# Kernel tuning notes

Measured on AMD Instinct MI355X. Metric: run time of the kernel, lower is better.

Reference implementation:

```python
import jax, jax.numpy as jnp
import numpy as np

BIG_NEG = -1000000000.0
B, N, X, D = 16, 32, 36, 2048
H = 512

def setup_inputs() -> dict:
    key = jax.random.key(0)
    ks = jax.random.split(key, 16)
    inp = {
        'fc_feats_target': jax.random.normal(ks[0], (B, 1, D), jnp.float32),
        'fc_feats_distr': jax.random.normal(ks[1], (B, N, D), jnp.float32),
        'att_feats_target': jax.random.normal(ks[2], (B, 1, X, D), jnp.float32),
        'att_feats_distr': jax.random.normal(ks[3], (B, N, X, D), jnp.float32),
        'att_masks_target': jax.random.randint(ks[4], (B, 1, X), 0, 2, jnp.int32),
        'att_masks_distr': jax.random.randint(ks[5], (B, N, X), 0, 2, jnp.int32),
        # scorer MLP params: Linear(2D->H), Linear(H->1)
        'W1': jax.random.normal(ks[6], (2 * D, H), jnp.float32) * 0.02,
        'b1': jnp.zeros((H,), jnp.float32),
        'W2': jax.random.normal(ks[7], (H, 1), jnp.float32) * 0.02,
        'b2': jnp.zeros((1,), jnp.float32),
        # bilinear weight, initialized to identity as in the module
        'Wbil': jnp.eye(D, dtype=jnp.float32),
        # object_scorer MLP params
        'oW1': jax.random.normal(ks[8], (2 * D, H), jnp.float32) * 0.02,
        'ob1': jnp.zeros((H,), jnp.float32),
        'oW2': jax.random.normal(ks[9], (H, 1), jnp.float32) * 0.02,
        'ob2': jnp.zeros((1,), jnp.float32),
    }
    return inp

def _mlp(x, W1, b1, W2, b2):
    h = jax.nn.relu(x @ W1 + b1)
    return (h @ W2 + b2)[..., 0]  # squeeze(-1)

def reference(fc_feats_target, fc_feats_distr, att_feats_target, att_feats_distr,
              att_masks_target, att_masks_distr,
              W1, b1, W2, b2, Wbil, oW1, ob1, oW2, ob2):
    # base scorer on global (fc) features
    ft = jnp.broadcast_to(fc_feats_target, fc_feats_distr.shape)  # [B,N,D]
    cat_feats = jnp.concatenate([ft, fc_feats_distr], axis=-1)    # [B,N,2D]
    scores = _mlp(cat_feats, W1, b1, W2, b2)                      # [B,N]

    # bilinear compatibility: einsum('bixd,biye,de->bixy') with target broadcast over i
    tproj = jnp.einsum('bxd,de->bxe', att_feats_target[:, 0], Wbil)        # [B,X,D]
    inners = jnp.einsum('bxd,biyd->bixy', tproj, att_feats_distr)          # [B,N,X,Y]

    mask_outer = (att_masks_target[:, 0][:, None, :, None]
                  * att_masks_distr[:, :, None, :])                        # [B,N,X,Y]
    inners = jnp.where(mask_outer > 0, inners, BIG_NEG)

    target_weights = jax.nn.softmax(jnp.max(inners, axis=3), axis=-1)      # [B,N,X]
    distr_weights = jax.nn.softmax(jnp.max(inners, axis=2), axis=-1)       # [B,N,Y]

    target_feats = jnp.einsum('bxd,bix->bid', att_feats_target[:, 0], target_weights)
    distr_feats = jnp.einsum('biyd,biy->bid', att_feats_distr, distr_weights)

    cat_att = jnp.concatenate([target_feats, distr_feats], axis=-1)        # [B,N,2D]
    scores = scores + _mlp(cat_att, oW1, ob1, oW2, ob2)

    return jax.nn.log_softmax(scores, axis=-1)  # [B,N]
```

## Files before the change

### kernel.cpp

```cpp
#include <hip/hip_runtime.h>
#include <math.h>

#define D_   2048
#define H_   512
#define K2D  4096
#define X_   36
#define NCOL 1152

#define Z_MLP 32
#define Z_TP  8
#define Z_S   4

#define O_A   0u
#define O_B   9437184u
#define O_SB  11534336u
#define O_SO  11534848u

#define SP_PLANE 663552u

typedef __attribute__((ext_vector_type(8))) short bf8_t;
typedef __attribute__((ext_vector_type(4))) float f4_t;

__device__ __forceinline__ unsigned short f2bf(float f) {
  unsigned u = __float_as_uint(f);
  unsigned r = u + 0x7FFFu + ((u >> 16) & 1u);
  return (unsigned short)(r >> 16);
}
__device__ __forceinline__ float bf2f(unsigned short h) {
  return __uint_as_float(((unsigned)h) << 16);
}

#define TSTR 40

__device__ __forceinline__ void cvt8(unsigned short* Hp, unsigned short* Lp,
                                     float4 a, float4 b) {
  __align__(16) unsigned short h[8], l[8];
  float x[8] = {a.x, a.y, a.z, a.w, b.x, b.y, b.z, b.w};
  #pragma unroll
  for (int j = 0; j < 8; j++) {
    h[j] = f2bf(x[j]);
    l[j] = f2bf(x[j] - bf2f(h[j]));
  }
  *(bf8_t*)Hp = *(bf8_t*)&h[0];
  *(bf8_t*)Lp = *(bf8_t*)&l[0];
}

__global__ __launch_bounds__(256, 4) void gemm_mfma64(
    const float* __restrict__ A, const float* __restrict__ A2,
    const float* __restrict__ Bm, float* __restrict__ Cpart,
    int M, int N, int K, int kchunk, int amode)
{
  __shared__ __align__(16) unsigned short AsH[64 * TSTR], AsL[64 * TSTR];
  __shared__ __align__(16) unsigned short BsH[64 * TSTR], BsL[64 * TSTR];
  const int t  = threadIdx.x;
  const int m0 = blockIdx.y << 6;
  const int n0 = blockIdx.x << 6;
  const int k0 = blockIdx.z * kchunk;
  const int kend = k0 + kchunk;
  const int w  = t >> 6;
  const int ln = t & 15;
  const int qd = (t >> 4) & 3;
  const int wm = (w >> 1) << 5;
  const int wn = (w & 1) << 5;
  const int a_row = t >> 2;
  const int a_kq  = (t & 3) << 3;
  const int b_col = t & 63;
  const int b_kq  = (t >> 6) << 3;

  f4_t acc[2][2];
  #pragma unroll
  for (int i = 0; i < 2; i++)
    #pragma unroll
    for (int j = 0; j < 2; j++) acc[i][j] = (f4_t)0.f;

  float4 pa0, pa1;
  float  pb[8];

  auto loadA = [&](int kb) {
    int gr = m0 + a_row;
    int gk = kb + a_kq;
    pa0 = make_float4(0.f, 0.f, 0.f, 0.f);
    pa1 = pa0;
    if (gr < M) {
      const float* src;
      if (amode == 0) src = A + (size_t)gr * K + gk;
      else src = (gk < 2048) ? (A  + ((size_t)(gr >> 5) << 11) + gk)
                             : (A2 + ((size_t)gr << 11) + (gk - 2048));
      pa0 = *(const float4*)src;
      pa1 = *(const float4*)(src + 4);
    }
  };
  auto loadB = [&](int kb) {
    #pragma unroll
    for (int j = 0; j < 8; j++)
      pb[j] = Bm[(size_t)(kb + b_kq + j) * N + n0 + b_col];
  };

  loadA(k0); loadB(k0);

  for (int kb = k0; kb < kend; kb += 32) {
    __syncthreads();
    cvt8(&AsH[a_row * TSTR + a_kq], &AsL[a_row * TSTR + a_kq], pa0, pa1);
    cvt8(&BsH[b_col * TSTR + b_kq], &BsL[b_col * TSTR + b_kq],
         make_float4(pb[0], pb[1], pb[2], pb[3]),
         make_float4(pb[4], pb[5], pb[6], pb[7]));
    __syncthreads();
    if (kb + 32 < kend) { loadA(kb + 32); loadB(kb + 32); }
    bf8_t ah[2], al[2], bh[2], bl[2];
    #pragma unroll
    for (int fm = 0; fm < 2; fm++) {
      int r = (wm + (fm << 4) + ln) * TSTR + (qd << 3);
      ah[fm] = *(const bf8_t*)&AsH[r];
      al[fm] = *(const bf8_t*)&AsL[r];
    }
    #pragma unroll
    for (int fn = 0; fn < 2; fn++) {
      int r = (wn + (fn << 4) + ln) * TSTR + (qd << 3);
      bh[fn] = *(const bf8_t*)&BsH[r];
      bl[fn] = *(const bf8_t*)&BsL[r];
    }
    #pragma unroll
    for (int fm = 0; fm < 2; fm++)
      #pragma unroll
      for (int fn = 0; fn < 2; fn++) {
        acc[fm][fn] = __builtin_amdgcn_mfma_f32_16x16x32_bf16(ah[fm], bh[fn], acc[fm][fn], 0, 0, 0);
        acc[fm][fn] = __builtin_amdgcn_mfma_f32_16x16x32_bf16(ah[fm], bl[fn], acc[fm][fn], 0, 0, 0);
        acc[fm][fn] = __builtin_amdgcn_mfma_f32_16x16x32_bf16(al[fm], bh[fn], acc[fm][fn], 0, 0, 0);
      }
  }
  float* Cz = Cpart + (size_t)blockIdx.z * M * N;
  #pragma unroll
  for (int fm = 0; fm < 2; fm++) {
    #pragma unroll
    for (int reg = 0; reg < 4; reg++) {
      int gr = m0 + wm + (fm << 4) + (qd << 2) + reg;
      if (gr < M) {
        #pragma unroll
        for (int fn = 0; fn < 2; fn++)
          Cz[(size_t)gr * N + n0 + wn + (fn << 4) + ln] = acc[fm][fn][reg];
      }
    }
  }
}

__global__ __launch_bounds__(256) void reduce_tp(
    const float* __restrict__ tpp, float* __restrict__ tproj)
{
  int idx = blockIdx.x * 256 + threadIdx.x;
  const float4* p = (const float4*)tpp;
  float4 a = p[idx];
  #pragma unroll
  for (int z = 1; z < Z_TP; z++) {
    float4 b = p[idx + (size_t)z * 294912];
    a.x += b.x; a.y += b.y; a.z += b.z; a.w += b.w;
  }
  ((float4*)tproj)[idx] = a;
}

__global__ __launch_bounds__(256, 4) void sgemm36_mfma(
    const float* __restrict__ tproj, const float* __restrict__ attd,
    float* __restrict__ Spart, int kchunk)
{
  __shared__ __align__(16) unsigned short AsH[48 * TSTR], AsL[48 * TSTR];
  __shared__ __align__(16) unsigned short BsH[64 * TSTR], BsL[64 * TSTR];
  const int t  = threadIdx.x;
  const int n0 = blockIdx.x << 6;
  const int b  = blockIdx.y;
  const int k0 = blockIdx.z * kchunk;
  const int kend = k0 + kchunk;
  const int w  = t >> 6;
  const int ln = t & 15;
  const int qd = (t >> 4) & 3;
  const float* Ab = tproj + (size_t)b * X_ * D_;
  const float* Bb = attd  + (size_t)b * NCOL * D_;
  const int a_row = t >> 2;
  const int a_kq  = (t & 3) << 3;
  const int b_col = t & 63;
  const int b_kq  = (t >> 6) << 3;

  f4_t acc[3];
  #pragma unroll
  for (int i = 0; i < 3; i++) acc[i] = (f4_t)0.f;

  float4 pa0, pa1, pb0, pb1;

  auto loadA = [&](int kb) {
    pa0 = make_float4(0.f, 0.f, 0.f, 0.f);
    pa1 = pa0;
    if (a_row < X_) {
      const float* src = Ab + (size_t)a_row * D_ + kb + a_kq;
      pa0 = *(const float4*)src;
      pa1 = *(const float4*)(src + 4);
    }
  };
  auto loadB = [&](int kb) {
    const float* src = Bb + (size_t)(n0 + b_col) * D_ + kb + b_kq;
    pb0 = *(const float4*)src;
    pb1 = *(const float4*)(src + 4);
  };

  loadA(k0); loadB(k0);

  for (int kb = k0; kb < kend; kb += 32) {
    __syncthreads();
    if (a_row < 48)
      cvt8(&AsH[a_row * TSTR + a_kq], &AsL[a_row * TSTR + a_kq], pa0, pa1);
    cvt8(&BsH[b_col * TSTR + b_kq], &BsL[b_col * TSTR + b_kq], pb0, pb1);
    __syncthreads();
    if (kb + 32 < kend) { loadA(kb + 32); loadB(kb + 32); }
    bf8_t ah[3], al[3], bh, bl;
    #pragma unroll
    for (int fm = 0; fm < 3; fm++) {
      int r = ((fm << 4) + ln) * TSTR + (qd << 3);
      ah[fm] = *(const bf8_t*)&AsH[r];
      al[fm] = *(const bf8_t*)&AsL[r];
    }
    {
      int r = ((w << 4) + ln) * TSTR + (qd << 3);
      bh = *(const bf8_t*)&BsH[r];
      bl = *(const bf8_t*)&BsL[r];
    }
    #pragma unroll
    for (int fm = 0; fm < 3; fm++) {
      acc[fm] = __builtin_amdgcn_mfma_f32_16x16x32_bf16(ah[fm], bh, acc[fm], 0, 0, 0);
      acc[fm] = __builtin_amdgcn_mfma_f32_16x16x32_bf16(ah[fm], bl, acc[fm], 0, 0, 0);
      acc[fm] = __builtin_amdgcn_mfma_f32_16x16x32_bf16(al[fm], bh, acc[fm], 0, 0, 0);
    }
  }
  float* Sz = Spart + (size_t)blockIdx.z * SP_PLANE + (size_t)b * X_ * NCOL;
  #pragma unroll
  for (int fm = 0; fm < 3; fm++) {
    #pragma unroll
    for (int reg = 0; reg < 4; reg++) {
      int x = (fm << 4) + (qd << 2) + reg;
      if (x < X_)
        Sz[(size_t)x * NCOL + n0 + (w << 4) + ln] = acc[fm][reg];
    }
  }
}

__global__ __launch_bounds__(256) void mlp_tail_z(
    const float* __restrict__ hp, const float* __restrict__ b1,
    const float* __restrict__ w2, const float* __restrict__ b2,
    float* __restrict__ out)
{
  int row = blockIdx.x;
  int t   = threadIdx.x;
  float v = 0.f;
  #pragma unroll
  for (int q = 0; q < 2; q++) {
    int h = t + (q << 8);
    float s = 0.f;
    #pragma unroll
    for (int z = 0; z < Z_MLP; z++)
      s += hp[(size_t)z * (H_ * 512) + (size_t)row * H_ + h];
    s += b1[h];
    v += fmaxf(s, 0.f) * w2[h];
  }
  #pragma unroll
  for (int off = 32; off > 0; off >>= 1) v += __shfl_down(v, off, 64);
  __shared__ float red[4];
  if ((t & 63) == 0) red[t >> 6] = v;
  __syncthreads();
  if (t == 0) out[row] = red[0] + red[1] + red[2] + red[3] + b2[0];
}

__global__ __launch_bounds__(256) void attn_fused(
    const float* __restrict__ Spart, const int* __restrict__ amt,
    const int* __restrict__ amd, const float* __restrict__ attt,
    const float* __restrict__ attd, float* __restrict__ cat)
{
  __shared__ float Sm[36 * 37];
  __shared__ int   mtv[36], mdv[36];
  __shared__ float mrow[36], mcol[36], twl[36], dwl[36];
  int bi = blockIdx.x;
  int b  = bi >> 5;
  int i  = bi & 31;
  int t  = threadIdx.x;
  if (t < 36) { mtv[t] = amt[b * 36 + t]; mdv[t] = amd[bi * 36 + t]; }
  __syncthreads();
  for (int f = t; f < 324; f += 256) {
    int x  = f / 9;
    int yq = (f - x * 9) << 2;
    size_t o = (((size_t)b * X_ + x) * NCOL + i * 36 + yq) >> 2;
    const float4* p = (const float4*)Spart;
    float4 v = p[o];
    #pragma unroll
    for (int z = 1; z < Z_S; z++) {
      float4 wv = p[o + ((size_t)z * SP_PLANE >> 2)];
      v.x += wv.x; v.y += wv.y; v.z += wv.z; v.w += wv.w;
    }
    float* dst = &Sm[x * 37 + yq];
    bool mx = (mtv[x] != 0);
    dst[0] = (mx && mdv[yq + 0] != 0) ? v.x : -1e9f;
    dst[1] = (mx && mdv[yq + 1] != 0) ? v.y : -1e9f;
    dst[2] = (mx && mdv[yq + 2] != 0) ? v.z : -1e9f;
    dst[3] = (mx && mdv[yq + 3] != 0) ? v.w : -1e9f;
  }
  __syncthreads();
  if (t < 36) {
    float r = -INFINITY, c = -INFINITY;
    for (int k = 0; k < 36; k++) {
      r = fmaxf(r, Sm[t * 37 + k]);
      c = fmaxf(c, Sm[k * 37 + t]);
    }
    mrow[t] = r; mcol[t] = c;
  }
  __syncthreads();
  if (t < 64) {
    float v = (t < 36) ? mrow[t] : -INFINITY;
    float m = v;
    #pragma unroll
    for (int off = 32; off > 0; off >>= 1) m = fmaxf(m, __shfl_xor(m, off, 64));
    float e = (t < 36) ? expf(v - m) : 0.f;
    float s = e;
    #pragma unroll
    for (int off = 32; off > 0; off >>= 1) s += __shfl_xor(s, off, 64);
    if (t < 36) twl[t] = e / s;
  } else if (t < 128) {
    int l = t - 64;
    float v = (l < 36) ? mcol[l] : -INFINITY;
    float m = v;
    #pragma unroll
    for (int off = 32; off > 0; off >>= 1) m = fmaxf(m, __shfl_xor(m, off, 64));
    float e = (l < 36) ? expf(v - m) : 0.f;
    float s = e;
    #pragma unroll
    for (int off = 32; off > 0; off >>= 1) s += __shfl_xor(s, off, 64);
    if (l < 36) dwl[l] = e / s;
  }
  __syncthreads();
  const float4* at4 = (const float4*)(attt + (size_t)b * X_ * D_);
  const float4* ad4 = (const float4*)(attd + (size_t)bi * X_ * D_);
  float4 t0 = make_float4(0, 0, 0, 0), t1 = t0, d0 = t0, d1 = t0;
  for (int x = 0; x < 36; x++) {
    float wt = twl[x], wd = dwl[x];
    float4 a  = at4[x * 512 + t];
    float4 a2 = at4[x * 512 + t + 256];
    float4 e  = ad4[x * 512 + t];
    float4 e2 = ad4[x * 512 + t + 256];
    t0.x = fmaf(wt, a.x, t0.x);  t0.y = fmaf(wt, a.y, t0.y);
    t0.z = fmaf(wt, a.z, t0.z);  t0.w = fmaf(wt, a.w, t0.w);
    t1.x = fmaf(wt, a2.x, t1.x); t1.y = fmaf(wt, a2.y, t1.y);
    t1.z = fmaf(wt, a2.z, t1.z); t1.w = fmaf(wt, a2.w, t1.w);
    d0.x = fmaf(wd, e.x, d0.x);  d0.y = fmaf(wd, e.y, d0.y);
    d0.z = fmaf(wd, e.z, d0.z);  d0.w = fmaf(wd, e.w, d0.w);
    d1.x = fmaf(wd, e2.x, d1.x); d1.y = fmaf(wd, e2.y, d1.y);
    d1.z = fmaf(wd, e2.z, d1.z); d1.w = fmaf(wd, e2.w, d1.w);
  }
  float4* c4 = (float4*)(cat + (size_t)bi * K2D);
  c4[t] = t0; c4[t + 256] = t1; c4[512 + t] = d0; c4[512 + t + 256] = d1;
}

__global__ __launch_bounds__(64) void lsm(
    const float* __restrict__ sb, const float* __restrict__ so,
    float* __restrict__ out)
{
  int b = blockIdx.x, t = threadIdx.x;
  float s = (t < 32) ? sb[b * 32 + t] + so[b * 32 + t] : -INFINITY;
  float m = s;
  #pragma unroll
  for (int off = 32; off > 0; off >>= 1) m = fmaxf(m, __shfl_xor(m, off, 64));
  float e = (t < 32) ? expf(s - m) : 0.f;
  float sum = e;
  #pragma unroll
  for (int off = 32; off > 0; off >>= 1) sum += __shfl_xor(sum, off, 64);
  if (t < 32) out[b * 32 + t] = s - m - logf(sum);
}

extern "C" void kernel_launch(void* const* d_in, const int* in_sizes, int n_in,
                              void* d_out, int out_size, void* d_ws, size_t ws_size,
                              hipStream_t stream)
{
  const float* fc_t  = (const float*)d_in[0];
  const float* fc_d  = (const float*)d_in[1];
  const float* att_t = (const float*)d_in[2];
  const float* att_d = (const float*)d_in[3];
  const int*   am_t  = (const int*)d_in[4];
  const int*   am_d  = (const int*)d_in[5];
  const float* W1    = (const float*)d_in[6];
  const float* b1    = (const float*)d_in[7];
  const float* W2    = (const float*)d_in[8];
  const float* b2    = (const float*)d_in[9];
  const float* Wbil  = (const float*)d_in[10];
  const float* oW1   = (const float*)d_in[11];
  const float* ob1   = (const float*)d_in[12];
  const float* oW2   = (const float*)d_in[13];
  const float* ob2   = (const float*)d_in[14];
  float* ws  = (float*)d_ws;
  float* out = (float*)d_out;

  gemm_mfma64<<<dim3(8, 8, Z_MLP), 256, 0, stream>>>(fc_t, fc_d, W1, ws + O_A,
                                                     512, 512, 4096, 4096 / Z_MLP, 1);
  mlp_tail_z<<<512, 256, 0, stream>>>(ws + O_A, b1, W2, b2, ws + O_SB);
  gemm_mfma64<<<dim3(32, 9, Z_TP), 256, 0, stream>>>(att_t, nullptr, Wbil, ws + O_A,
                                                     576, 2048, 2048, 2048 / Z_TP, 0);
  reduce_tp<<<1152, 256, 0, stream>>>(ws + O_A, ws + O_B);
  sgemm36_mfma<<<dim3(18, 16, Z_S), 256, 0, stream>>>(ws + O_B, att_d, ws + O_A,
                                                      2048 / Z_S);
  attn_fused<<<512, 256, 0, stream>>>(ws + O_A, am_t, am_d, att_t, att_d, ws + O_B);
  gemm_mfma64<<<dim3(8, 8, Z_MLP), 256, 0, stream>>>(ws + O_B, nullptr, oW1, ws + O_A,
                                                     512, 512, 4096, 4096 / Z_MLP, 0);
  mlp_tail_z<<<512, 256, 0, stream>>>(ws + O_A, ob1, oW2, ob2, ws + O_SO);
  lsm<<<16, 64, 0, stream>>>(ws + O_SB, ws + O_SO, out);
}
```

Before: 389.3 us.

## Fuse per-pair bilinear score GEMM into attention kernel and pre-split tproj to bf16

Replaces the split-K sgemm36 kernel plus its partial-sum workspace with a fused kernel that computes each (b,i) 36x36 score tile in LDS via bf16x3 MFMA and then does the masked max/softmax/weighted-sum in the same block. The tproj reduction now also emits hi/lo bf16 splits padded to 48 rows, so the fused kernel skips converting A. Split-K factors for the MLP and tproj GEMMs are lowered, which cuts partial-sum traffic. In exchange, each fused block runs a full K=2048 loop serially over only 512 blocks, and tproj is re-read once per i.

```diff
diff --git a/kernel.cpp b/kernel.cpp
--- a/kernel.cpp
+++ b/kernel.cpp
@@ -7,16 +7,15 @@
 #define X_   36
 #define NCOL 1152
 
-#define Z_MLP 32
-#define Z_TP  8
-#define Z_S   4
-
-#define O_A   0u
-#define O_B   9437184u
-#define O_SB  11534336u
-#define O_SO  11534848u
-
-#define SP_PLANE 663552u
+#define Z_MLP 8
+#define Z_TP  4
+
+#define O_A    0u
+#define O_TPH  4718592u
+#define O_TPL  5505024u
+#define O_CAT  6291456u
+#define O_SB   8388608u
+#define O_SO   8389120u
 
 typedef __attribute__((ext_vector_type(8))) short bf8_t;
 typedef __attribute__((ext_vector_type(4))) float f4_t;
@@ -30,8 +29,6 @@
   return __uint_as_float(((unsigned)h) << 16);
 }
 
-#define TSTR 40
-
 __device__ __forceinline__ void cvt8(unsigned short* Hp, unsigned short* Lp,
                                      float4 a, float4 b) {
   __align__(16) unsigned short h[8], l[8];
@@ -44,6 +41,8 @@
   *(bf8_t*)Hp = *(bf8_t*)&h[0];
   *(bf8_t*)Lp = *(bf8_t*)&l[0];
 }
+
+#define TSTR 40
 
 __global__ __launch_bounds__(256, 4) void gemm_mfma64(
     const float* __restrict__ A, const float* __restrict__ A2,
@@ -143,159 +142,123 @@
   }
 }
 
-__global__ __launch_bounds__(256) void reduce_tp(
-    const float* __restrict__ tpp, float* __restrict__ tproj)
-{
-  int idx = blockIdx.x * 256 + threadIdx.x;
-  const float4* p = (const float4*)tpp;
-  float4 a = p[idx];
-  #pragma unroll
-  for (int z = 1; z < Z_TP; z++) {
-    float4 b = p[idx + (size_t)z * 294912];
-    a.x += b.x; a.y += b.y; a.z += b.z; a.w += b.w;
-  }
-  ((float4*)tproj)[idx] = a;
-}
-
-__global__ __launch_bounds__(256, 4) void sgemm36_mfma(
-    const float* __restrict__ tproj, const float* __restrict__ attd,
-    float* __restrict__ Spart, int kchunk)
-{
-  __shared__ __align__(16) unsigned short AsH[48 * TSTR], AsL[48 * TSTR];
-  __shared__ __align__(16) unsigned short BsH[64 * TSTR], BsL[64 * TSTR];
-  const int t  = threadIdx.x;
-  const int n0 = blockIdx.x << 6;
-  const int b  = blockIdx.y;
-  const int k0 = blockIdx.z * kchunk;
-  const int kend = k0 + kchunk;
-  const int w  = t >> 6;
-  const int ln = t & 15;
-  const int qd = (t >> 4) & 3;
-  const float* Ab = tproj + (size_t)b * X_ * D_;
-  const float* Bb = attd  + (size_t)b * NCOL * D_;
-  const int a_row = t >> 2;
-  const int a_kq  = (t & 3) << 3;
-  const int b_col = t & 63;
-  const int b_kq  = (t >> 6) << 3;
-
-  f4_t acc[3];
-  #pragma unroll
-  for (int i = 0; i < 3; i++) acc[i] = (f4_t)0.f;
-
-  float4 pa0, pa1, pb0, pb1;
-
-  auto loadA = [&](int kb) {
-    pa0 = make_float4(0.f, 0.f, 0.f, 0.f);
-    pa1 = pa0;
-    if (a_row < X_) {
-      const float* src = Ab + (size_t)a_row * D_ + kb + a_kq;
-      pa0 = *(const float4*)src;
-      pa1 = *(const float4*)(src + 4);
-    }
-  };
-  auto loadB = [&](int kb) {
-    const float* src = Bb + (size_t)(n0 + b_col) * D_ + kb + b_kq;
-    pb0 = *(const float4*)src;
-    pb1 = *(const float4*)(src + 4);
-  };
-
-  loadA(k0); loadB(k0);
-
-  for (int kb = k0; kb < kend; kb += 32) {
-    __syncthreads();
-    if (a_row < 48)
-      cvt8(&AsH[a_row * TSTR + a_kq], &AsL[a_row * TSTR + a_kq], pa0, pa1);
-    cvt8(&BsH[b_col * TSTR + b_kq], &BsL[b_col * TSTR + b_kq], pb0, pb1);
-    __syncthreads();
-    if (kb + 32 < kend) { loadA(kb + 32); loadB(kb + 32); }
-    bf8_t ah[3], al[3], bh, bl;
-    #pragma unroll
-    for (int fm = 0; fm < 3; fm++) {
-      int r = ((fm << 4) + ln) * TSTR + (qd << 3);
-      ah[fm] = *(const bf8_t*)&AsH[r];
-      al[fm] = *(const bf8_t*)&AsL[r];
-    }
-    {
-      int r = ((w << 4) + ln) * TSTR + (qd << 3);
-      bh = *(const bf8_t*)&BsH[r];
-      bl = *(const bf8_t*)&BsL[r];
-    }
-    #pragma unroll
-    for (int fm = 0; fm < 3; fm++) {
-      acc[fm] = __builtin_amdgcn_mfma_f32_16x16x32_bf16(ah[fm], bh, acc[fm], 0, 0, 0);
-      acc[fm] = __builtin_amdgcn_mfma_f32_16x16x32_bf16(ah[fm], bl, acc[fm], 0, 0, 0);
-      acc[fm] = __builtin_amdgcn_mfma_f32_16x16x32_bf16(al[fm], bh, acc[fm], 0, 0, 0);
-    }
-  }
-  float* Sz = Spart + (size_t)blockIdx.z * SP_PLANE + (size_t)b * X_ * NCOL;
-  #pragma unroll
-  for (int fm = 0; fm < 3; fm++) {
-    #pragma unroll
-    for (int reg = 0; reg < 4; reg++) {
-      int x = (fm << 4) + (qd << 2) + reg;
-      if (x < X_)
-        Sz[(size_t)x * NCOL + n0 + (w << 4) + ln] = acc[fm][reg];
-    }
-  }
-}
-
-__global__ __launch_bounds__(256) void mlp_tail_z(
-    const float* __restrict__ hp, const float* __restrict__ b1,
-    const float* __restrict__ w2, const float* __restrict__ b2,
-    float* __restrict__ out)
-{
-  int row = blockIdx.x;
-  int t   = threadIdx.x;
-  float v = 0.f;
-  #pragma unroll
-  for (int q = 0; q < 2; q++) {
-    int h = t + (q << 8);
-    float s = 0.f;
-    #pragma unroll
-    for (int z = 0; z < Z_MLP; z++)
-      s += hp[(size_t)z * (H_ * 512) + (size_t)row * H_ + h];
-    s += b1[h];
-    v += fmaxf(s, 0.f) * w2[h];
-  }
-  #pragma unroll
-  for (int off = 32; off > 0; off >>= 1) v += __shfl_down(v, off, 64);
-  __shared__ float red[4];
-  if ((t & 63) == 0) red[t >> 6] = v;
-  __syncthreads();
-  if (t == 0) out[row] = red[0] + red[1] + red[2] + red[3] + b2[0];
-}
-
-__global__ __launch_bounds__(256) void attn_fused(
-    const float* __restrict__ Spart, const int* __restrict__ amt,
+__global__ __launch_bounds__(256) void reduce_tp_bf(
+    const float* __restrict__ tpp, unsigned short* __restrict__ tph,
+    unsigned short* __restrict__ tpl)
+{
+  int blk = blockIdx.x;
+  int b = blk / 48, row = blk - b * 48;
+  int t = threadIdx.x;
+  size_t obase = (size_t)(b * 48 + row) * 2048;
+  if (row < X_) {
+    size_t ibase = (size_t)(b * X_ + row) * 2048;
+    #pragma unroll
+    for (int q = 0; q < 8; q++) {
+      int c = t + (q << 8);
+      float v = tpp[ibase + c];
+      #pragma unroll
+      for (int z = 1; z < Z_TP; z++) v += tpp[(size_t)z * 1179648 + ibase + c];
+      unsigned short h = f2bf(v);
+      tph[obase + c] = h;
+      tpl[obase + c] = f2bf(v - bf2f(h));
+    }
+  } else {
+    #pragma unroll
+    for (int q = 0; q < 8; q++) {
+      int c = t + (q << 8);
+      tph[obase + c] = 0; tpl[obase + c] = 0;
+    }
+  }
+}
+
+#define SROW 136
+
+__global__ __launch_bounds__(256, 2) void fused_si(
+    const unsigned short* __restrict__ tph, const unsigned short* __restrict__ tpl,
+    const float* __restrict__ attd, const int* __restrict__ amt,
     const int* __restrict__ amd, const float* __restrict__ attt,
-    const float* __restrict__ attd, float* __restrict__ cat)
-{
+    float* __restrict__ cat)
+{
+  __shared__ __align__(16) char sbuf[4 * 48 * SROW * 2];
   __shared__ float Sm[36 * 37];
   __shared__ int   mtv[36], mdv[36];
   __shared__ float mrow[36], mcol[36], twl[36], dwl[36];
-  int bi = blockIdx.x;
-  int b  = bi >> 5;
-  int i  = bi & 31;
-  int t  = threadIdx.x;
+  unsigned short* AH = (unsigned short*)sbuf;
+  unsigned short* AL = AH + 48 * SROW;
+  unsigned short* BH = AL + 48 * SROW;
+  unsigned short* BL = BH + 48 * SROW;
+  const int bi = blockIdx.x, b = bi >> 5, i = bi & 31;
+  const int t = threadIdx.x;
+  const int w = t >> 6, ln = t & 15, qd = (t >> 4) & 3;
   if (t < 36) { mtv[t] = amt[b * 36 + t]; mdv[t] = amd[bi * 36 + t]; }
-  __syncthreads();
-  for (int f = t; f < 324; f += 256) {
-    int x  = f / 9;
-    int yq = (f - x * 9) << 2;
-    size_t o = (((size_t)b * X_ + x) * NCOL + i * 36 + yq) >> 2;
-    const float4* p = (const float4*)Spart;
-    float4 v = p[o];
-    #pragma unroll
-    for (int z = 1; z < Z_S; z++) {
-      float4 wv = p[o + ((size_t)z * SP_PLANE >> 2)];
-      v.x += wv.x; v.y += wv.y; v.z += wv.z; v.w += wv.w;
-    }
-    float* dst = &Sm[x * 37 + yq];
-    bool mx = (mtv[x] != 0);
-    dst[0] = (mx && mdv[yq + 0] != 0) ? v.x : -1e9f;
-    dst[1] = (mx && mdv[yq + 1] != 0) ? v.y : -1e9f;
-    dst[2] = (mx && mdv[yq + 2] != 0) ? v.z : -1e9f;
-    dst[3] = (mx && mdv[yq + 3] != 0) ? v.w : -1e9f;
+
+  const unsigned short* Ah = tph + (size_t)b * 48 * 2048;
+  const unsigned short* Al = tpl + (size_t)b * 48 * 2048;
+  const float* Bb = attd + (size_t)bi * X_ * D_;
+
+  f4_t acc[3][3];
+  #pragma unroll
+  for (int fm = 0; fm < 3; fm++)
+    #pragma unroll
+    for (int fn = 0; fn < 3; fn++) acc[fm][fn] = (f4_t)0.f;
+
+  for (int c = 0; c < 16; c++) {
+    int kb = c << 7;
+    __syncthreads();
+    #pragma unroll
+    for (int j = 0; j < 3; j++) {
+      int u = t + (j << 8);
+      int row = u >> 4, ks = (u & 15) << 3;
+      *(bf8_t*)&AH[row * SROW + ks] = *(const bf8_t*)&Ah[(size_t)row * 2048 + kb + ks];
+      *(bf8_t*)&AL[row * SROW + ks] = *(const bf8_t*)&Al[(size_t)row * 2048 + kb + ks];
+      if (row < X_) {
+        const float* src = Bb + (size_t)row * D_ + kb + ks;
+        cvt8(&BH[row * SROW + ks], &BL[row * SROW + ks],
+             *(const float4*)src, *(const float4*)(src + 4));
+      } else {
+        *(bf8_t*)&BH[row * SROW + ks] = (bf8_t)(short)0;
+        *(bf8_t*)&BL[row * SROW + ks] = (bf8_t)(short)0;
+      }
+    }
+    __syncthreads();
+    const int ks = (w << 5) + (qd << 3);
+    bf8_t ah[3], al[3], bh[3], bl[3];
+    #pragma unroll
+    for (int f = 0; f < 3; f++) {
+      int r = ((f << 4) + ln) * SROW + ks;
+      ah[f] = *(const bf8_t*)&AH[r];
+      al[f] = *(const bf8_t*)&AL[r];
+      bh[f] = *(const bf8_t*)&BH[r];
+      bl[f] = *(const bf8_t*)&BL[r];
+    }
+    #pragma unroll
+    for (int fm = 0; fm < 3; fm++)
+      #pragma unroll
+      for (int fn = 0; fn < 3; fn++) {
+        acc[fm][fn] = __builtin_amdgcn_mfma_f32_16x16x32_bf16(ah[fm], bh[fn], acc[fm][fn], 0, 0, 0);
+        acc[fm][fn] = __builtin_amdgcn_mfma_f32_16x16x32_bf16(ah[fm], bl[fn], acc[fm][fn], 0, 0, 0);
+        acc[fm][fn] = __builtin_amdgcn_mfma_f32_16x16x32_bf16(al[fm], bh[fn], acc[fm][fn], 0, 0, 0);
+      }
+  }
+  __syncthreads();
+  float* Sp = (float*)sbuf + w * 2304;
+  #pragma unroll
+  for (int fm = 0; fm < 3; fm++)
+    #pragma unroll
+    for (int reg = 0; reg < 4; reg++) {
+      int row = (fm << 4) + (qd << 2) + reg;
+      #pragma unroll
+      for (int fn = 0; fn < 3; fn++)
+        Sp[row * 48 + (fn << 4) + ln] = acc[fm][fn][reg];
+    }
+  __syncthreads();
+  const float* S0 = (const float*)sbuf;
+  for (int u = t; u < 2304; u += 256) {
+    int row = u / 48, col = u - row * 48;
+    if (row < X_ && col < X_) {
+      float v = S0[u] + S0[u + 2304] + S0[u + 4608] + S0[u + 6912];
+      Sm[row * 37 + col] = (mtv[row] != 0 && mdv[col] != 0) ? v : -1e9f;
+    }
   }
   __syncthreads();
   if (t < 36) {
@@ -352,6 +315,32 @@
   c4[t] = t0; c4[t + 256] = t1; c4[512 + t] = d0; c4[512 + t + 256] = d1;
 }
 
+__global__ __launch_bounds__(256) void mlp_tail_z(
+    const float* __restrict__ hp, const float* __restrict__ b1,
+    const float* __restrict__ w2, const float* __restrict__ b2,
+    float* __restrict__ out)
+{
+  int row = blockIdx.x;
+  int t   = threadIdx.x;
+  float v = 0.f;
+  #pragma unroll
+  for (int q = 0; q < 2; q++) {
+    int h = t + (q << 8);
+    float s = 0.f;
+    #pragma unroll
+    for (int z = 0; z < Z_MLP; z++)
+      s += hp[(size_t)z * (H_ * 512) + (size_t)row * H_ + h];
+    s += b1[h];
+    v += fmaxf(s, 0.f) * w2[h];
+  }
+  #pragma unroll
+  for (int off = 32; off > 0; off >>= 1) v += __shfl_down(v, off, 64);
+  __shared__ float red[4];
+  if ((t & 63) == 0) red[t >> 6] = v;
+  __syncthreads();
+  if (t == 0) out[row] = red[0] + red[1] + red[2] + red[3] + b2[0];
+}
+
 __global__ __launch_bounds__(64) void lsm(
     const float* __restrict__ sb, const float* __restrict__ so,
     float* __restrict__ out)
@@ -395,11 +384,13 @@
   mlp_tail_z<<<512, 256, 0, stream>>>(ws + O_A, b1, W2, b2, ws + O_SB);
   gemm_mfma64<<<dim3(32, 9, Z_TP), 256, 0, stream>>>(att_t, nullptr, Wbil, ws + O_A,
                                                      576, 2048, 2048, 2048 / Z_TP, 0);
-  reduce_tp<<<1152, 256, 0, stream>>>(ws + O_A, ws + O_B);
-  sgemm36_mfma<<<dim3(18, 16, Z_S), 256, 0, stream>>>(ws + O_B, att_d, ws + O_A,
-                                                      2048 / Z_S);
-  attn_fused<<<512, 256, 0, stream>>>(ws + O_A, am_t, am_d, att_t, att_d, ws + O_B);
-  gemm_mfma64<<<dim3(8, 8, Z_MLP), 256, 0, stream>>>(ws + O_B, nullptr, oW1, ws + O_A,
+  reduce_tp_bf<<<768, 256, 0, stream>>>(ws + O_A,
+                                        (unsigned short*)(ws + O_TPH),
+                                        (unsigned short*)(ws + O_TPL));
+  fused_si<<<512, 256, 0, stream>>>((const unsigned short*)(ws + O_TPH),
+                                    (const unsigned short*)(ws + O_TPL),
+                                    att_d, am_t, am_d, att_t, ws + O_CAT);
+  gemm_mfma64<<<dim3(8, 8, Z_MLP), 256, 0, stream>>>(ws + O_CAT, nullptr, oW1, ws + O_A,
                                                      512, 512, 4096, 4096 / Z_MLP, 0);
   mlp_tail_z<<<512, 256, 0, stream>>>(ws + O_A, ob1, oW2, ob2, ws + O_SO);
   lsm<<<16, 64, 0, stream>>>(ws + O_SB, ws + O_SO, out);
```

Measured after the change: 395.0 us. No clear change (+1.5%).
